# Optimization experiments

Hardware: AMD Instinct MI355X
Metric: run time of the kernel (lower is better)

## Reference

```python
import jax, jax.numpy as jnp
import numpy as np

N_NODES = 100000

def gcn_conv(x, edge_index, W, b):
    # GCNConv with normalize=True and self-loops:
    # out = D^{-1/2} (A + I) D^{-1/2} (x W) + b
    h = x @ W                                   # [N, out]
    src, dst = edge_index[0], edge_index[1]
    deg = jax.ops.segment_sum(jnp.ones(src.shape[0], h.dtype), dst,
                              num_segments=N_NODES) + 1.0  # +1 for self loop
    dinv = jax.lax.rsqrt(deg)
    norm = dinv[src] * dinv[dst]                # [E]
    agg = jax.ops.segment_sum(h[src] * norm[:, None], dst,
                              num_segments=N_NODES)        # [N, out]
    agg = agg + h * (1.0 / deg)[:, None]        # self-loop term: norm_ii = 1/deg_i
    return agg + b


def setup_inputs() -> dict:
    key = jax.random.key(0)
    k0, k1, k2, k3 = jax.random.split(key, 4)
    N, E, F_IN, H, C = N_NODES, 1600000, 256, 128, 40
    x = jax.random.normal(k0, (N, F_IN), dtype=jnp.float32)
    edge_index = jax.random.randint(k1, (2, E), 0, N, dtype=jnp.int64)
    W1 = jax.random.normal(k2, (F_IN, H), dtype=jnp.float32) * (1.0 / np.sqrt(F_IN))
    b1 = jnp.zeros((H,), jnp.float32)
    W2 = jax.random.normal(k3, (H, C), dtype=jnp.float32) * (1.0 / np.sqrt(H))
    b2 = jnp.zeros((C,), jnp.float32)
    return {"x": x, "edge_index": edge_index, "W1": W1, "b1": b1, "W2": W2, "b2": b2}


def reference(x, edge_index, W1, b1, W2, b2):
    # layer 1 + ReLU (dropout = identity in eval mode)
    h = jax.nn.relu(gcn_conv(x, edge_index, W1, b1))
    # final layer (no activation)
    return gcn_conv(h, edge_index, W2, b2)
```

## Files before the change

kernel.cpp:

```cpp
#include <hip/hip_runtime.h>
#include <hip/hip_bf16.h>


#define FIN 256
#define HDIM 128
#define CDIM 40
#define CAP 8192
#define EC 8192

typedef __attribute__((ext_vector_type(8))) short bf16x8;
typedef __attribute__((ext_vector_type(4))) float f32x4;
typedef __attribute__((ext_vector_type(2))) float f32x2;

__device__ inline short f2bf(float f) {
    unsigned u = __float_as_uint(f);
    unsigned r = (u + 0x7FFFu + ((u >> 16) & 1u)) >> 16;
    return (short)r;
}
__device__ inline float bflo(unsigned u) { return __uint_as_float(u << 16); }
__device__ inline float bfhi(unsigned u) { return __uint_as_float(u & 0xFFFF0000u); }
__device__ inline f32x2 unpk(unsigned u) { return (f32x2){bflo(u), bfhi(u)}; }
__device__ inline float ub0(unsigned u) { return (float)(u & 255u); }
__device__ inline float ub1(unsigned u) { return (float)((u >> 8) & 255u); }
__device__ inline float ub2(unsigned u) { return (float)((u >> 16) & 255u); }
__device__ inline float ub3(unsigned u) { return (float)(u >> 24); }

__global__ __launch_bounds__(1024) void scatter_k(const int* __restrict__ ei, int* __restrict__ gcnt,
                                                  int* __restrict__ bmem, int E, int NBUCK) {
    __shared__ int hist[512];
    __shared__ int base[512];
    const int tid = threadIdx.x;
    for (int t = tid; t < NBUCK; t += 1024) hist[t] = 0;
    __syncthreads();
    const int e0 = blockIdx.x * EC;
    const int e1 = min(E, e0 + EC);
    for (int e = e0 + tid; e < e1; e += 1024) atomicAdd(&hist[ei[E + e] >> 8], 1);
    __syncthreads();
    for (int t = tid; t < NBUCK; t += 1024) base[t] = atomicAdd(&gcnt[t], hist[t]);
    __syncthreads();
    for (int e = e0 + tid; e < e1; e += 1024) {
        int s = ei[e];
        int d = ei[E + e];
        int b = d >> 8;
        int pos = atomicAdd(&base[b], 1);
        bmem[b * CAP + pos] = s | ((d & 255) << 20);
    }
}

__global__ __launch_bounds__(256) void p2_build_k(const int* __restrict__ bmem, const int* __restrict__ bcnt,
                                                  int* __restrict__ csr, int2* __restrict__ nseg,
                                                  float* __restrict__ dinv, float* __restrict__ invd,
                                                  const float* __restrict__ W1, const float* __restrict__ W2,
                                                  short* __restrict__ W1T, short* __restrict__ W2T, int N) {
    __shared__ int hist[256], cur[256], sc[256];
    __shared__ int stage[CAP];
    const int b = blockIdx.x;
    const int tid = threadIdx.x;

    for (int idx = b * 256 + tid; idx < FIN * HDIM + 48 * HDIM; idx += gridDim.x * 256) {
        if (idx < FIN * HDIM) {
            int k = idx >> 7, n = idx & 127;
            W1T[n * FIN + k] = f2bf(W1[idx]);
        } else {
            int j = idx - FIN * HDIM;
            int c = j >> 7, k = j & 127;
            W2T[j] = (c < CDIM) ? f2bf(W2[k * CDIM + c]) : (short)0;
        }
    }

    int cnt = bcnt[b];
    if (cnt > CAP) cnt = CAP;
    const int* src = bmem + b * CAP;
    hist[tid] = 0;
    __syncthreads();
    for (int j = tid; j < cnt; j += 256) atomicAdd(&hist[src[j] >> 20], 1);
    __syncthreads();
    int v = hist[tid];
    sc[tid] = v;
    __syncthreads();
    for (int off = 1; off < 256; off <<= 1) {
        int t = (tid >= off) ? sc[tid - off] : 0;
        __syncthreads();
        sc[tid] += t;
        __syncthreads();
    }
    int excl = sc[tid] - v;
    cur[tid] = excl;
    int i = b * 256 + tid;
    if (i < N) {
        nseg[i] = make_int2(b * CAP + excl, v);
        float dg = (float)(v + 1);
        dinv[i] = rsqrtf(dg);
        invd[i] = 1.0f / dg;
    }
    __syncthreads();
    for (int j = tid; j < cnt; j += 256) {
        int rec = src[j];
        int pos = atomicAdd(&cur[rec >> 20], 1);
        stage[pos] = rec & 0xFFFFF;
    }
    __syncthreads();
    int* dst = csr + b * CAP;
    for (int j = tid; j < cnt; j += 256) dst[j] = stage[j];
}

#define LDSTRIDE 40
__global__ __launch_bounds__(256) void gemm1_mfma_k(const float* __restrict__ X,
                                                    const short* __restrict__ W1T,
                                                    const float* __restrict__ dinv,
                                                    unsigned char* __restrict__ T1q,
                                                    float* __restrict__ scl,
                                                    float* __restrict__ wsc, int N) {
    __shared__ short SH[128 * LDSTRIDE * 2];
    short* As = SH;
    short* Bs = SH + 128 * LDSTRIDE;
    const int tid = threadIdx.x;
    const int lane = tid & 63;
    const int wid = tid >> 6;
    const int w0 = wid & 1, w1 = wid >> 1;
    const int quad = lane >> 4;
    const int l16 = lane & 15;
    const int rowbase = blockIdx.x * 128;
    const int sr = tid >> 1;
    const int sh = tid & 1;

    f32x4 acc[4][4];
#pragma unroll
    for (int a = 0; a < 4; a++)
#pragma unroll
        for (int b = 0; b < 4; b++) acc[a][b] = (f32x4){0.f, 0.f, 0.f, 0.f};

    const int arow = min(rowbase + sr, N - 1);
    const float* xsrc = X + (size_t)arow * FIN + sh * 16;
    const int4* bsrc = (const int4*)(W1T + (size_t)sr * FIN + sh * 16);

    for (int k0 = 0; k0 < FIN; k0 += 32) {
        float vals[16];
        *(float4*)&vals[0]  = *(const float4*)(xsrc + k0);
        *(float4*)&vals[4]  = *(const float4*)(xsrc + k0 + 4);
        *(float4*)&vals[8]  = *(const float4*)(xsrc + k0 + 8);
        *(float4*)&vals[12] = *(const float4*)(xsrc + k0 + 12);
        short tmp[16];
#pragma unroll
        for (int c = 0; c < 16; c++) tmp[c] = f2bf(vals[c]);
        ((int4*)&As[sr * LDSTRIDE + sh * 16])[0] = ((int4*)tmp)[0];
        ((int4*)&As[sr * LDSTRIDE + sh * 16])[1] = ((int4*)tmp)[1];
        int4 b0 = bsrc[k0 >> 3];
        int4 b1 = bsrc[(k0 >> 3) + 1];
        ((int4*)&Bs[sr * LDSTRIDE + sh * 16])[0] = b0;
        ((int4*)&Bs[sr * LDSTRIDE + sh * 16])[1] = b1;
        __syncthreads();

        bf16x8 afr[4], bfr[4];
#pragma unroll
        for (int mt = 0; mt < 4; mt++)
            afr[mt] = *(const bf16x8*)&As[(w1 * 64 + mt * 16 + l16) * LDSTRIDE + quad * 8];
#pragma unroll
        for (int nt = 0; nt < 4; nt++)
            bfr[nt] = *(const bf16x8*)&Bs[(w0 * 64 + nt * 16 + l16) * LDSTRIDE + quad * 8];
#pragma unroll
        for (int mt = 0; mt < 4; mt++)
#pragma unroll
            for (int nt = 0; nt < 4; nt++)
                acc[mt][nt] = __builtin_amdgcn_mfma_f32_16x16x32_bf16(afr[mt], bfr[nt], acc[mt][nt], 0, 0, 0);
        __syncthreads();
    }

    unsigned char* qbuf = (unsigned char*)SH;
    float* rmaxb = (float*)((char*)SH + 16384);
#pragma unroll
    for (int mt = 0; mt < 4; mt++) {
#pragma unroll
        for (int r = 0; r < 4; r++) {
            float m = fabsf(acc[mt][0][r]);
            m = fmaxf(m, fabsf(acc[mt][1][r]));
            m = fmaxf(m, fabsf(acc[mt][2][r]));
            m = fmaxf(m, fabsf(acc[mt][3][r]));
#pragma unroll
            for (int off = 1; off < 16; off <<= 1) m = fmaxf(m, __shfl_xor(m, off));
            rmaxb[w0 * 128 + w1 * 64 + mt * 16 + quad * 4 + r] = m;
        }
    }
    __syncthreads();
    if (tid < 128) {
        int grow = rowbase + tid;
        if (grow < N) {
            float rv = fmaxf(rmaxb[tid], rmaxb[128 + tid]);
            float s = rv * (1.f / 127.f);
            scl[grow] = s;
            wsc[grow] = s * dinv[grow];
        }
    }
#pragma unroll
    for (int mt = 0; mt < 4; mt++) {
#pragma unroll
        for (int r = 0; r < 4; r++) {
            const int row = w1 * 64 + mt * 16 + quad * 4 + r;
            float rv = fmaxf(rmaxb[row], rmaxb[128 + row]);
            float qinv = rv > 0.f ? 127.f / rv : 0.f;
#pragma unroll
            for (int nt = 0; nt < 4; nt++) {
                int qi = (int)rintf(acc[mt][nt][r] * qinv) + 128;
                qi = qi < 0 ? 0 : (qi > 255 ? 255 : qi);
                qbuf[row * 128 + w0 * 64 + nt * 16 + l16] = (unsigned char)qi;
            }
        }
    }
    __syncthreads();
#pragma unroll
    for (int it = 0; it < 4; it++) {
        int idx = tid + it * 256;
        int row = idx >> 3;
        if (rowbase + row < N)
            ((uint4*)(T1q + (size_t)(rowbase + row) * 128))[idx & 7] = ((const uint4*)qbuf)[idx];
    }
}

__global__ __launch_bounds__(256) void agg1_k(const unsigned char* __restrict__ T1q, const int2* __restrict__ nseg,
                                              const int* __restrict__ csr, const float* __restrict__ wsc,
                                              const float* __restrict__ scl, const float* __restrict__ dinv,
                                              const float* __restrict__ invd, const float* __restrict__ b1,
                                              unsigned* __restrict__ Hb, int N) {
    const int lane = threadIdx.x & 63;
    const int quad = lane >> 4;
    const int ql = lane & 15;
    const int i = blockIdx.x * 4 + (threadIdx.x >> 6);
    if (i >= N) return;
    const int2 sg = nseg[i];
    const int e0 = sg.x, deg = sg.y;
    int sv = 0; float wv = 0.f;
    if (lane < deg) { sv = csr[e0 + lane]; wv = wsc[sv]; }

    const uint2* rowp = (const uint2*)T1q;
    uint2 us = rowp[i * 16 + ql];
    const float sscale = scl[i];

    f32x2 acc[4]; float asum = 0.f;
#pragma unroll
    for (int t = 0; t < 4; t++) acc[t] = (f32x2){0.f, 0.f};

    const int dmain = deg < 64 ? deg : 64;
    for (int j = 0; j < dmain; j += 16) {
        const int i0 = j + quad, i1 = j + 4 + quad, i2 = j + 8 + quad, i3 = j + 12 + quad;
        int s0 = __shfl(sv, i0); int s1 = __shfl(sv, i1);
        int s2 = __shfl(sv, i2); int s3 = __shfl(sv, i3);
        float w0 = __shfl(wv, i0); float w1 = __shfl(wv, i1);
        float w2 = __shfl(wv, i2); float w3 = __shfl(wv, i3);
        w0 = (i0 < dmain) ? w0 : 0.f;
        w1 = (i1 < dmain) ? w1 : 0.f;
        w2 = (i2 < dmain) ? w2 : 0.f;
        w3 = (i3 < dmain) ? w3 : 0.f;
        uint2 u0 = rowp[s0 * 16 + ql];
        uint2 u1 = rowp[s1 * 16 + ql];
        uint2 u2 = rowp[s2 * 16 + ql];
        uint2 u3 = rowp[s3 * 16 + ql];
        asum += w0 + w1 + w2 + w3;
        f32x2 W0 = (f32x2){w0, w0}, W1v = (f32x2){w1, w1}, W2v = (f32x2){w2, w2}, W3v = (f32x2){w3, w3};
        acc[0] += W0 * (f32x2){ub0(u0.x), ub1(u0.x)} + W1v * (f32x2){ub0(u1.x), ub1(u1.x)}
                + W2v * (f32x2){ub0(u2.x), ub1(u2.x)} + W3v * (f32x2){ub0(u3.x), ub1(u3.x)};
        acc[1] += W0 * (f32x2){ub2(u0.x), ub3(u0.x)} + W1v * (f32x2){ub2(u1.x), ub3(u1.x)}
                + W2v * (f32x2){ub2(u2.x), ub3(u2.x)} + W3v * (f32x2){ub2(u3.x), ub3(u3.x)};
        acc[2] += W0 * (f32x2){ub0(u0.y), ub1(u0.y)} + W1v * (f32x2){ub0(u1.y), ub1(u1.y)}
                + W2v * (f32x2){ub0(u2.y), ub1(u2.y)} + W3v * (f32x2){ub0(u3.y), ub1(u3.y)};
        acc[3] += W0 * (f32x2){ub2(u0.y), ub3(u0.y)} + W1v * (f32x2){ub2(u1.y), ub3(u1.y)}
                + W2v * (f32x2){ub2(u2.y), ub3(u2.y)} + W3v * (f32x2){ub2(u3.y), ub3(u3.y)};
    }
    const int eEnd = e0 + deg;
    for (int e = e0 + 64; e < eEnd; e += 4) {
        int idx = e + quad;
        int cl = idx < eEnd ? idx : eEnd - 1;
        int sj = csr[cl];
        float wj = (idx < eEnd) ? wsc[sj] : 0.f;
        uint2 u = rowp[sj * 16 + ql];
        asum += wj;
        f32x2 Wj = (f32x2){wj, wj};
        acc[0] += Wj * (f32x2){ub0(u.x), ub1(u.x)};
        acc[1] += Wj * (f32x2){ub2(u.x), ub3(u.x)};
        acc[2] += Wj * (f32x2){ub0(u.y), ub1(u.y)};
        acc[3] += Wj * (f32x2){ub2(u.y), ub3(u.y)};
    }
#pragma unroll
    for (int t = 0; t < 4; t++) {
        acc[t].x += __shfl_xor(acc[t].x, 16); acc[t].y += __shfl_xor(acc[t].y, 16);
        acc[t].x += __shfl_xor(acc[t].x, 32); acc[t].y += __shfl_xor(acc[t].y, 32);
    }
    asum += __shfl_xor(asum, 16);
    asum += __shfl_xor(asum, 32);

    const float di = dinv[i];
    const float sf2 = invd[i] * sscale;
    const float K = -128.f * (sf2 + di * asum);
    float4 bA = *(const float4*)(b1 + ql * 8);
    float4 bB = *(const float4*)(b1 + ql * 8 + 4);
    float o0 = fmaxf(bA.x + sf2 * ub0(us.x) + di * acc[0].x + K, 0.f);
    float o1 = fmaxf(bA.y + sf2 * ub1(us.x) + di * acc[0].y + K, 0.f);
    float o2 = fmaxf(bA.z + sf2 * ub2(us.x) + di * acc[1].x + K, 0.f);
    float o3 = fmaxf(bA.w + sf2 * ub3(us.x) + di * acc[1].y + K, 0.f);
    float o4 = fmaxf(bB.x + sf2 * ub0(us.y) + di * acc[2].x + K, 0.f);
    float o5 = fmaxf(bB.y + sf2 * ub1(us.y) + di * acc[2].y + K, 0.f);
    float o6 = fmaxf(bB.z + sf2 * ub2(us.y) + di * acc[3].x + K, 0.f);
    float o7 = fmaxf(bB.w + sf2 * ub3(us.y) + di * acc[3].y + K, 0.f);
    uint4 pk;
    pk.x = ((unsigned)(unsigned short)f2bf(o0)) | (((unsigned)(unsigned short)f2bf(o1)) << 16);
    pk.y = ((unsigned)(unsigned short)f2bf(o2)) | (((unsigned)(unsigned short)f2bf(o3)) << 16);
    pk.z = ((unsigned)(unsigned short)f2bf(o4)) | (((unsigned)(unsigned short)f2bf(o5)) << 16);
    pk.w = ((unsigned)(unsigned short)f2bf(o6)) | (((unsigned)(unsigned short)f2bf(o7)) << 16);
    if (quad == 0) ((uint4*)(Hb + (size_t)i * 64))[ql] = pk;
}

__global__ __launch_bounds__(256) void gemm2_mfma_k(const short* __restrict__ Hb,
                                                    const short* __restrict__ W2T,
                                                    const float* __restrict__ dinv,
                                                    unsigned char* __restrict__ T2q,
                                                    float* __restrict__ scl2,
                                                    float* __restrict__ wsc2, int N) {
    __shared__ short As[128 * LDSTRIDE];
    __shared__ short Bs[48 * LDSTRIDE];
    const int tid = threadIdx.x;
    const int lane = tid & 63;
    const int wid = tid >> 6;
    const int quad = lane >> 4;
    const int l16 = lane & 15;
    const int rowbase = blockIdx.x * 128;
    const int sr = tid >> 1;
    const int sh = tid & 1;

    f32x4 acc[2][3];
#pragma unroll
    for (int a = 0; a < 2; a++)
#pragma unroll
        for (int b = 0; b < 3; b++) acc[a][b] = (f32x4){0.f, 0.f, 0.f, 0.f};

    const int arow = min(rowbase + sr, N - 1);
    const int4* asrc = (const int4*)(Hb + (size_t)arow * HDIM + sh * 16);
    const int br = tid >> 1, bh = tid & 1;
    const int4* bsrc = (const int4*)(W2T + br * HDIM + bh * 16);

    for (int k0 = 0; k0 < HDIM; k0 += 32) {
        int4 a0 = asrc[k0 >> 3];
        int4 a1 = asrc[(k0 >> 3) + 1];
        ((int4*)&As[sr * LDSTRIDE + sh * 16])[0] = a0;
        ((int4*)&As[sr * LDSTRIDE + sh * 16])[1] = a1;
        if (tid < 96) {
            int4 b0 = bsrc[k0 >> 3];
            int4 b1 = bsrc[(k0 >> 3) + 1];
            ((int4*)&Bs[br * LDSTRIDE + bh * 16])[0] = b0;
            ((int4*)&Bs[br * LDSTRIDE + bh * 16])[1] = b1;
        }
        __syncthreads();
        bf16x8 afr[2], bfr[3];
#pragma unroll
        for (int mt = 0; mt < 2; mt++)
            afr[mt] = *(const bf16x8*)&As[(wid * 32 + mt * 16 + l16) * LDSTRIDE + quad * 8];
#pragma unroll
        for (int nt = 0; nt < 3; nt++)
            bfr[nt] = *(const bf16x8*)&Bs[(nt * 16 + l16) * LDSTRIDE + quad * 8];
#pragma unroll
        for (int mt = 0; mt < 2; mt++)
#pragma unroll
            for (int nt = 0; nt < 3; nt++)
                acc[mt][nt] = __builtin_amdgcn_mfma_f32_16x16x32_bf16(afr[mt], bfr[nt], acc[mt][nt], 0, 0, 0);
        __syncthreads();
    }

    unsigned char* qbuf = (unsigned char*)As;
#pragma unroll
    for (int mt = 0; mt < 2; mt++) {
#pragma unroll
        for (int r = 0; r < 4; r++) {
            float m = fmaxf(fmaxf(fabsf(acc[mt][0][r]), fabsf(acc[mt][1][r])), fabsf(acc[mt][2][r]));
#pragma unroll
            for (int off = 1; off < 16; off <<= 1) m = fmaxf(m, __shfl_xor(m, off));
            const int row = wid * 32 + mt * 16 + quad * 4 + r;
            const int grow = rowbase + row;
            const float qinv = m > 0.f ? 127.f / m : 0.f;
            if (l16 == 0 && grow < N) {
                float s = m * (1.f / 127.f);
                scl2[grow] = s;
                wsc2[grow] = s * dinv[grow];
            }
            int q0 = (int)rintf(acc[mt][0][r] * qinv) + 128;
            int q1 = (int)rintf(acc[mt][1][r] * qinv) + 128;
            int q2 = (int)rintf(acc[mt][2][r] * qinv) + 128;
            q0 = q0 < 0 ? 0 : (q0 > 255 ? 255 : q0);
            q1 = q1 < 0 ? 0 : (q1 > 255 ? 255 : q1);
            q2 = q2 < 0 ? 0 : (q2 > 255 ? 255 : q2);
            qbuf[row * 64 + l16]      = (unsigned char)q0;
            qbuf[row * 64 + 16 + l16] = (unsigned char)q1;
            qbuf[row * 64 + 32 + l16] = (unsigned char)q2;
        }
    }
    for (int idx = tid; idx < 2048; idx += 256)
        qbuf[(idx >> 4) * 64 + 48 + (idx & 15)] = (unsigned char)128;
    __syncthreads();
#pragma unroll
    for (int it = 0; it < 2; it++) {
        int idx = tid + it * 256;
        int row = idx >> 2;
        if (rowbase + row < N)
            ((uint4*)(T2q + (size_t)(rowbase + row) * 64))[idx & 3] = ((const uint4*)qbuf)[idx];
    }
}

__global__ __launch_bounds__(256) void agg2_k(const unsigned char* __restrict__ T2q, const int2* __restrict__ nseg,
                                              const int* __restrict__ csr, const float* __restrict__ wsc2,
                                              const float* __restrict__ scl2, const float* __restrict__ dinv,
                                              const float* __restrict__ invd, const float* __restrict__ b2,
                                              float* __restrict__ OUT, int N) {
    const int lane = threadIdx.x & 63;
    const int oct = lane >> 3;
    const int olr = lane & 7;
    const int i = blockIdx.x * 4 + (threadIdx.x >> 6);
    if (i >= N) return;
    const int2 sg = nseg[i];
    const int e0 = sg.x, deg = sg.y;
    int sv = 0; float wv = 0.f;
    if (lane < deg) { sv = csr[e0 + lane]; wv = wsc2[sv]; }

    const uint2* rowp = (const uint2*)T2q;
    uint2 us = rowp[i * 8 + olr];
    const float sscale = scl2[i];

    f32x2 acc[4]; float asum = 0.f;
#pragma unroll
    for (int t = 0; t < 4; t++) acc[t] = (f32x2){0.f, 0.f};

    const int dmain = deg < 64 ? deg : 64;
    for (int j = 0; j < dmain; j += 16) {
        const int i0 = j + oct, i1 = j + 8 + oct;
        int s0 = __shfl(sv, i0); int s1 = __shfl(sv, i1);
        float w0 = __shfl(wv, i0); float w1 = __shfl(wv, i1);
        w0 = (i0 < dmain) ? w0 : 0.f;
        w1 = (i1 < dmain) ? w1 : 0.f;
        uint2 u0 = rowp[s0 * 8 + olr];
        uint2 u1 = rowp[s1 * 8 + olr];
        asum += w0 + w1;
        f32x2 W0 = (f32x2){w0, w0}, W1v = (f32x2){w1, w1};
        acc[0] += W0 * (f32x2){ub0(u0.x), ub1(u0.x)} + W1v * (f32x2){ub0(u1.x), ub1(u1.x)};
        acc[1] += W0 * (f32x2){ub2(u0.x), ub3(u0.x)} + W1v * (f32x2){ub2(u1.x), ub3(u1.x)};
        acc[2] += W0 * (f32x2){ub0(u0.y), ub1(u0.y)} + W1v * (f32x2){ub0(u1.y), ub1(u1.y)};
        acc[3] += W0 * (f32x2){ub2(u0.y), ub3(u0.y)} + W1v * (f32x2){ub2(u1.y), ub3(u1.y)};
    }
    const int eEnd = e0 + deg;
    for (int e = e0 + 64; e < eEnd; e += 8) {
        int idx = e + oct;
        int cl = idx < eEnd ? idx : eEnd - 1;
        int sj = csr[cl];
        float wj = (idx < eEnd) ? wsc2[sj] : 0.f;
        uint2 u = rowp[sj * 8 + olr];
        asum += wj;
        f32x2 Wj = (f32x2){wj, wj};
        acc[0] += Wj * (f32x2){ub0(u.x), ub1(u.x)};
        acc[1] += Wj * (f32x2){ub2(u.x), ub3(u.x)};
        acc[2] += Wj * (f32x2){ub0(u.y), ub1(u.y)};
        acc[3] += Wj * (f32x2){ub2(u.y), ub3(u.y)};
    }
#pragma unroll
    for (int t = 0; t < 4; t++) {
        acc[t].x += __shfl_xor(acc[t].x, 8);  acc[t].y += __shfl_xor(acc[t].y, 8);
        acc[t].x += __shfl_xor(acc[t].x, 16); acc[t].y += __shfl_xor(acc[t].y, 16);
        acc[t].x += __shfl_xor(acc[t].x, 32); acc[t].y += __shfl_xor(acc[t].y, 32);
    }
    asum += __shfl_xor(asum, 8);
    asum += __shfl_xor(asum, 16);
    asum += __shfl_xor(asum, 32);

    if (oct == 0 && olr < 5) {
        const float di = dinv[i];
        const float sf2 = invd[i] * sscale;
        const float K = -128.f * (sf2 + di * asum);
        float4 bA = *(const float4*)(b2 + olr * 8);
        float4 bB = *(const float4*)(b2 + olr * 8 + 4);
        float4 oA, oB;
        oA.x = bA.x + sf2 * ub0(us.x) + di * acc[0].x + K;
        oA.y = bA.y + sf2 * ub1(us.x) + di * acc[0].y + K;
        oA.z = bA.z + sf2 * ub2(us.x) + di * acc[1].x + K;
        oA.w = bA.w + sf2 * ub3(us.x) + di * acc[1].y + K;
        oB.x = bB.x + sf2 * ub0(us.y) + di * acc[2].x + K;
        oB.y = bB.y + sf2 * ub1(us.y) + di * acc[2].y + K;
        oB.z = bB.z + sf2 * ub2(us.y) + di * acc[3].x + K;
        oB.w = bB.w + sf2 * ub3(us.y) + di * acc[3].y + K;
        *(float4*)(OUT + (size_t)i * CDIM + olr * 8) = oA;
        *(float4*)(OUT + (size_t)i * CDIM + olr * 8 + 4) = oB;
    }
}

extern "C" void kernel_launch(void* const* d_in, const int* in_sizes, int n_in,
                              void* d_out, int out_size, void* d_ws, size_t ws_size,
                              hipStream_t stream) {
    const float* x   = (const float*)d_in[0];
    const int*   ei  = (const int*)d_in[1];
    const float* W1  = (const float*)d_in[2];
    const float* b1  = (const float*)d_in[3];
    const float* W2  = (const float*)d_in[4];
    const float* b2  = (const float*)d_in[5];
    float*       out = (float*)d_out;

    const int Hd  = in_sizes[3];
    const int Fin = in_sizes[2] / Hd;
    const int N   = in_sizes[0] / Fin;
    const int E   = in_sizes[1] / 2;

    const int NBUCK = (N + 255) / 256;
    const int NB1   = (E + EC - 1) / EC;

    char* base = (char*)d_ws;
    size_t off = 0;
    auto alloc = [&](size_t bytes) -> void* {
        void* p = base + off;
        off += (bytes + 255) & ~(size_t)255;
        return p;
    };
    size_t bmemB = (size_t)NBUCK * CAP * 4;
    size_t t1qB  = (size_t)N * 128;
    size_t regA  = bmemB > t1qB ? bmemB : t1qB;
    char* pA = (char*)alloc(regA);
    int*           bmem = (int*)pA;
    unsigned char* t1q  = (unsigned char*)pA;

    int*      gcnt = (int*)alloc((size_t)NBUCK * 4);
    int*      csr  = (int*)alloc((size_t)NBUCK * CAP * 4);
    int2*     nseg = (int2*)alloc((size_t)N * 8);
    float*    dinv = (float*)alloc((size_t)N * 4);
    float*    invd = (float*)alloc((size_t)N * 4);
    float*    scl  = (float*)alloc((size_t)N * 4);
    float*    wsc  = (float*)alloc((size_t)N * 4);
    float*    scl2 = (float*)alloc((size_t)N * 4);
    float*    wsc2 = (float*)alloc((size_t)N * 4);
    short*    W1T  = (short*)alloc((size_t)HDIM * FIN * 2);
    short*    W2T  = (short*)alloc((size_t)48 * HDIM * 2);
    unsigned* hb   = (unsigned*)alloc((size_t)N * HDIM * 2);
    unsigned char* t2q = (unsigned char*)alloc((size_t)N * 64);

    hipMemsetAsync(gcnt, 0, (size_t)NBUCK * 4, stream);
    scatter_k<<<NB1, 1024, 0, stream>>>(ei, gcnt, bmem, E, NBUCK);
    p2_build_k<<<NBUCK, 256, 0, stream>>>(bmem, gcnt, csr, nseg, dinv, invd, W1, W2, W1T, W2T, N);

    gemm1_mfma_k<<<(N + 127) / 128, 256, 0, stream>>>(x, W1T, dinv, t1q, scl, wsc, N);
    agg1_k<<<(N + 3) / 4, 256, 0, stream>>>(t1q, nseg, csr, wsc, scl, dinv, invd, b1, hb, N);
    gemm2_mfma_k<<<(N + 127) / 128, 256, 0, stream>>>((const short*)hb, W2T, dinv, t2q, scl2, wsc2, N);
    agg2_k<<<(N + 3) / 4, 256, 0, stream>>>(t2q, nseg, csr, wsc2, scl2, dinv, invd, b2, out, N);
}
```

Before: 326.1 us.

## Replace bucketed CSR build with global degree count, scan, and atomic fill

Replaces the two-pass bucketed scatter (fixed-capacity per-bucket staging plus an LDS sort) with three simpler kernels. The first counts degrees with global atomics, the second does a per-block scan with an atomic global offset, and the third fills the CSR with per-destination atomic cursors. This removes the capacity-limited staging buffer and its extra read/write pass, at the cost of many global atomics and a neighbor order within each row that is no longer deterministic. The row order now depends on block completion order, which changes memory locality for the aggregation kernels. The GEMM1 fp32-to-bf16 conversion also switches to the packed intrinsic.

```diff
diff --git a/kernel.cpp b/kernel.cpp
--- a/kernel.cpp
+++ b/kernel.cpp
@@ -5,8 +5,6 @@
 #define FIN 256
 #define HDIM 128
 #define CDIM 40
-#define CAP 8192
-#define EC 8192
 
 typedef __attribute__((ext_vector_type(8))) short bf16x8;
 typedef __attribute__((ext_vector_type(4))) float f32x4;
@@ -25,35 +23,18 @@
 __device__ inline float ub2(unsigned u) { return (float)((u >> 16) & 255u); }
 __device__ inline float ub3(unsigned u) { return (float)(u >> 24); }
 
-__global__ __launch_bounds__(1024) void scatter_k(const int* __restrict__ ei, int* __restrict__ gcnt,
-                                                  int* __restrict__ bmem, int E, int NBUCK) {
-    __shared__ int hist[512];
-    __shared__ int base[512];
-    const int tid = threadIdx.x;
-    for (int t = tid; t < NBUCK; t += 1024) hist[t] = 0;
-    __syncthreads();
-    const int e0 = blockIdx.x * EC;
-    const int e1 = min(E, e0 + EC);
-    for (int e = e0 + tid; e < e1; e += 1024) atomicAdd(&hist[ei[E + e] >> 8], 1);
-    __syncthreads();
-    for (int t = tid; t < NBUCK; t += 1024) base[t] = atomicAdd(&gcnt[t], hist[t]);
-    __syncthreads();
-    for (int e = e0 + tid; e < e1; e += 1024) {
-        int s = ei[e];
-        int d = ei[E + e];
-        int b = d >> 8;
-        int pos = atomicAdd(&base[b], 1);
-        bmem[b * CAP + pos] = s | ((d & 255) << 20);
-    }
-}
-
-__global__ __launch_bounds__(256) void p2_build_k(const int* __restrict__ bmem, const int* __restrict__ bcnt,
-                                                  int* __restrict__ csr, int2* __restrict__ nseg,
-                                                  float* __restrict__ dinv, float* __restrict__ invd,
-                                                  const float* __restrict__ W1, const float* __restrict__ W2,
-                                                  short* __restrict__ W1T, short* __restrict__ W2T, int N) {
-    __shared__ int hist[256], cur[256], sc[256];
-    __shared__ int stage[CAP];
+__global__ __launch_bounds__(1024) void deg_k(const int* __restrict__ ei, int* __restrict__ deg, int E) {
+    int e = blockIdx.x * 1024 + threadIdx.x;
+    if (e < E) atomicAdd(&deg[ei[E + e]], 1);
+}
+
+__global__ __launch_bounds__(256) void alloc_k(const int* __restrict__ deg, int* __restrict__ total,
+                                               int2* __restrict__ nseg, int* __restrict__ cur,
+                                               float* __restrict__ dinv, float* __restrict__ invd,
+                                               const float* __restrict__ W1, const float* __restrict__ W2,
+                                               short* __restrict__ W1T, short* __restrict__ W2T, int N) {
+    __shared__ int sc[256];
+    __shared__ int bbase;
     const int b = blockIdx.x;
     const int tid = threadIdx.x;
 
@@ -68,14 +49,8 @@
         }
     }
 
-    int cnt = bcnt[b];
-    if (cnt > CAP) cnt = CAP;
-    const int* src = bmem + b * CAP;
-    hist[tid] = 0;
-    __syncthreads();
-    for (int j = tid; j < cnt; j += 256) atomicAdd(&hist[src[j] >> 20], 1);
-    __syncthreads();
-    int v = hist[tid];
+    const int i = b * 256 + tid;
+    const int v = (i < N) ? deg[i] : 0;
     sc[tid] = v;
     __syncthreads();
     for (int off = 1; off < 256; off <<= 1) {
@@ -84,24 +59,29 @@
         sc[tid] += t;
         __syncthreads();
     }
-    int excl = sc[tid] - v;
-    cur[tid] = excl;
-    int i = b * 256 + tid;
+    const int incl = sc[tid];
+    const int excl = incl - v;
+    if (tid == 255) bbase = atomicAdd(total, incl);
+    __syncthreads();
+    const int base = bbase;
     if (i < N) {
-        nseg[i] = make_int2(b * CAP + excl, v);
+        nseg[i] = make_int2(base + excl, v);
+        cur[i] = base + excl;
         float dg = (float)(v + 1);
         dinv[i] = rsqrtf(dg);
         invd[i] = 1.0f / dg;
     }
-    __syncthreads();
-    for (int j = tid; j < cnt; j += 256) {
-        int rec = src[j];
-        int pos = atomicAdd(&cur[rec >> 20], 1);
-        stage[pos] = rec & 0xFFFFF;
-    }
-    __syncthreads();
-    int* dst = csr + b * CAP;
-    for (int j = tid; j < cnt; j += 256) dst[j] = stage[j];
+}
+
+__global__ __launch_bounds__(1024) void fill_k(const int* __restrict__ ei, int* __restrict__ cur,
+                                               int* __restrict__ csr, int E) {
+    int e = blockIdx.x * 1024 + threadIdx.x;
+    if (e < E) {
+        int s = ei[e];
+        int d = ei[E + e];
+        int pos = atomicAdd(&cur[d], 1);
+        csr[pos] = s;
+    }
 }
 
 #define LDSTRIDE 40
@@ -140,11 +120,12 @@
         *(float4*)&vals[4]  = *(const float4*)(xsrc + k0 + 4);
         *(float4*)&vals[8]  = *(const float4*)(xsrc + k0 + 8);
         *(float4*)&vals[12] = *(const float4*)(xsrc + k0 + 12);
-        short tmp[16];
-#pragma unroll
-        for (int c = 0; c < 16; c++) tmp[c] = f2bf(vals[c]);
-        ((int4*)&As[sr * LDSTRIDE + sh * 16])[0] = ((int4*)tmp)[0];
-        ((int4*)&As[sr * LDSTRIDE + sh * 16])[1] = ((int4*)tmp)[1];
+        __hip_bfloat162 tmp2[8];
+#pragma unroll
+        for (int c = 0; c < 8; c++)
+            tmp2[c] = __float22bfloat162_rn(make_float2(vals[2 * c], vals[2 * c + 1]));
+        ((int4*)&As[sr * LDSTRIDE + sh * 16])[0] = ((int4*)tmp2)[0];
+        ((int4*)&As[sr * LDSTRIDE + sh * 16])[1] = ((int4*)tmp2)[1];
         int4 b0 = bsrc[k0 >> 3];
         int4 b1 = bsrc[(k0 >> 3) + 1];
         ((int4*)&Bs[sr * LDSTRIDE + sh * 16])[0] = b0;
@@ -502,7 +483,7 @@
     const int E   = in_sizes[1] / 2;
 
     const int NBUCK = (N + 255) / 256;
-    const int NB1   = (E + EC - 1) / EC;
+    const int NBE   = (E + 1023) / 1024;
 
     char* base = (char*)d_ws;
     size_t off = 0;
@@ -511,15 +492,10 @@
         off += (bytes + 255) & ~(size_t)255;
         return p;
     };
-    size_t bmemB = (size_t)NBUCK * CAP * 4;
-    size_t t1qB  = (size_t)N * 128;
-    size_t regA  = bmemB > t1qB ? bmemB : t1qB;
-    char* pA = (char*)alloc(regA);
-    int*           bmem = (int*)pA;
-    unsigned char* t1q  = (unsigned char*)pA;
-
-    int*      gcnt = (int*)alloc((size_t)NBUCK * 4);
-    int*      csr  = (int*)alloc((size_t)NBUCK * CAP * 4);
+    unsigned char* t1q  = (unsigned char*)alloc((size_t)N * 128);
+    int*      deg  = (int*)alloc(((size_t)N + 64) * 4);
+    int*      cur  = (int*)alloc((size_t)N * 4);
+    int*      csr  = (int*)alloc((size_t)E * 4);
     int2*     nseg = (int2*)alloc((size_t)N * 8);
     float*    dinv = (float*)alloc((size_t)N * 4);
     float*    invd = (float*)alloc((size_t)N * 4);
@@ -531,10 +507,12 @@
     short*    W2T  = (short*)alloc((size_t)48 * HDIM * 2);
     unsigned* hb   = (unsigned*)alloc((size_t)N * HDIM * 2);
     unsigned char* t2q = (unsigned char*)alloc((size_t)N * 64);
-
-    hipMemsetAsync(gcnt, 0, (size_t)NBUCK * 4, stream);
-    scatter_k<<<NB1, 1024, 0, stream>>>(ei, gcnt, bmem, E, NBUCK);
-    p2_build_k<<<NBUCK, 256, 0, stream>>>(bmem, gcnt, csr, nseg, dinv, invd, W1, W2, W1T, W2T, N);
+    int* total = deg + N;
+
+    hipMemsetAsync(deg, 0, ((size_t)N + 64) * 4, stream);
+    deg_k<<<NBE, 1024, 0, stream>>>(ei, deg, E);
+    alloc_k<<<NBUCK, 256, 0, stream>>>(deg, total, nseg, cur, dinv, invd, W1, W2, W1T, W2T, N);
+    fill_k<<<NBE, 1024, 0, stream>>>(ei, cur, csr, E);
 
     gemm1_mfma_k<<<(N + 127) / 128, 256, 0, stream>>>(x, W1T, dinv, t1q, scl, wsc, N);
     agg1_k<<<(N + 3) / 4, 256, 0, stream>>>(t1q, nseg, csr, wsc, scl, dinv, invd, b1, hb, N);
```

Measured after the change: 470.8 us. 44.4% more time.

## Regroup agg2 lanes to 16 per row with 4-byte loads; use bf16x2 conversion

Applied to the files above, without the earlier changes.

The layer-2 aggregation kernel now assigns 16 lanes per neighbor row, each loading 4 bytes of the 64-byte quantized row, so one wavefront processes four neighbors per step instead of eight lanes per row with 8-byte loads. This changes how many rows are gathered concurrently, halves the per-lane accumulators and drops one shuffle-reduction stage. Separately, the GEMM's fp32-to-bf16 conversion now uses the paired __float22bfloat162_rn intrinsic instead of manual per-element rounding, which may map to a packed convert instruction. Narrower per-lane loads mean more load instructions per byte gathered.

```diff
diff --git a/kernel.cpp b/kernel.cpp
--- a/kernel.cpp
+++ b/kernel.cpp
@@ -140,11 +140,12 @@
         *(float4*)&vals[4]  = *(const float4*)(xsrc + k0 + 4);
         *(float4*)&vals[8]  = *(const float4*)(xsrc + k0 + 8);
         *(float4*)&vals[12] = *(const float4*)(xsrc + k0 + 12);
-        short tmp[16];
-#pragma unroll
-        for (int c = 0; c < 16; c++) tmp[c] = f2bf(vals[c]);
-        ((int4*)&As[sr * LDSTRIDE + sh * 16])[0] = ((int4*)tmp)[0];
-        ((int4*)&As[sr * LDSTRIDE + sh * 16])[1] = ((int4*)tmp)[1];
+        __hip_bfloat162 tmp2[8];
+#pragma unroll
+        for (int c = 0; c < 8; c++)
+            tmp2[c] = __float22bfloat162_rn(make_float2(vals[2 * c], vals[2 * c + 1]));
+        ((int4*)&As[sr * LDSTRIDE + sh * 16])[0] = ((int4*)tmp2)[0];
+        ((int4*)&As[sr * LDSTRIDE + sh * 16])[1] = ((int4*)tmp2)[1];
         int4 b0 = bsrc[k0 >> 3];
         int4 b1 = bsrc[(k0 >> 3) + 1];
         ((int4*)&Bs[sr * LDSTRIDE + sh * 16])[0] = b0;
@@ -408,8 +409,8 @@
                                               const float* __restrict__ invd, const float* __restrict__ b2,
                                               float* __restrict__ OUT, int N) {
     const int lane = threadIdx.x & 63;
-    const int oct = lane >> 3;
-    const int olr = lane & 7;
+    const int quad = lane >> 4;
+    const int ql = lane & 15;
     const int i = blockIdx.x * 4 + (threadIdx.x >> 6);
     if (i >= N) return;
     const int2 sg = nseg[i];
@@ -417,71 +418,67 @@
     int sv = 0; float wv = 0.f;
     if (lane < deg) { sv = csr[e0 + lane]; wv = wsc2[sv]; }
 
-    const uint2* rowp = (const uint2*)T2q;
-    uint2 us = rowp[i * 8 + olr];
+    const unsigned* rowp = (const unsigned*)T2q;
+    unsigned us = rowp[i * 16 + ql];
     const float sscale = scl2[i];
 
-    f32x2 acc[4]; float asum = 0.f;
-#pragma unroll
-    for (int t = 0; t < 4; t++) acc[t] = (f32x2){0.f, 0.f};
+    f32x2 acc[2]; float asum = 0.f;
+    acc[0] = (f32x2){0.f, 0.f};
+    acc[1] = (f32x2){0.f, 0.f};
 
     const int dmain = deg < 64 ? deg : 64;
     for (int j = 0; j < dmain; j += 16) {
-        const int i0 = j + oct, i1 = j + 8 + oct;
+        const int i0 = j + quad, i1 = j + 4 + quad, i2 = j + 8 + quad, i3 = j + 12 + quad;
         int s0 = __shfl(sv, i0); int s1 = __shfl(sv, i1);
+        int s2 = __shfl(sv, i2); int s3 = __shfl(sv, i3);
         float w0 = __shfl(wv, i0); float w1 = __shfl(wv, i1);
+        float w2 = __shfl(wv, i2); float w3 = __shfl(wv, i3);
         w0 = (i0 < dmain) ? w0 : 0.f;
         w1 = (i1 < dmain) ? w1 : 0.f;
-        uint2 u0 = rowp[s0 * 8 + olr];
-        uint2 u1 = rowp[s1 * 8 + olr];
-        asum += w0 + w1;
-        f32x2 W0 = (f32x2){w0, w0}, W1v = (f32x2){w1, w1};
-        acc[0] += W0 * (f32x2){ub0(u0.x), ub1(u0.x)} + W1v * (f32x2){ub0(u1.x), ub1(u1.x)};
-        acc[1] += W0 * (f32x2){ub2(u0.x), ub3(u0.x)} + W1v * (f32x2){ub2(u1.x), ub3(u1.x)};
-        acc[2] += W0 * (f32x2){ub0(u0.y), ub1(u0.y)} + W1v * (f32x2){ub0(u1.y), ub1(u1.y)};
-        acc[3] += W0 * (f32x2){ub2(u0.y), ub3(u0.y)} + W1v * (f32x2){ub2(u1.y), ub3(u1.y)};
+        w2 = (i2 < dmain) ? w2 : 0.f;
+        w3 = (i3 < dmain) ? w3 : 0.f;
+        unsigned u0 = rowp[s0 * 16 + ql];
+        unsigned u1 = rowp[s1 * 16 + ql];
+        unsigned u2 = rowp[s2 * 16 + ql];
+        unsigned u3 = rowp[s3 * 16 + ql];
+        asum += w0 + w1 + w2 + w3;
+        f32x2 W0 = (f32x2){w0, w0}, W1v = (f32x2){w1, w1}, W2v = (f32x2){w2, w2}, W3v = (f32x2){w3, w3};
+        acc[0] += W0 * (f32x2){ub0(u0), ub1(u0)} + W1v * (f32x2){ub0(u1), ub1(u1)}
+                + W2v * (f32x2){ub0(u2), ub1(u2)} + W3v * (f32x2){ub0(u3), ub1(u3)};
+        acc[1] += W0 * (f32x2){ub2(u0), ub3(u0)} + W1v * (f32x2){ub2(u1), ub3(u1)}
+                + W2v * (f32x2){ub2(u2), ub3(u2)} + W3v * (f32x2){ub2(u3), ub3(u3)};
     }
     const int eEnd = e0 + deg;
-    for (int e = e0 + 64; e < eEnd; e += 8) {
-        int idx = e + oct;
+    for (int e = e0 + 64; e < eEnd; e += 4) {
+        int idx = e + quad;
         int cl = idx < eEnd ? idx : eEnd - 1;
         int sj = csr[cl];
         float wj = (idx < eEnd) ? wsc2[sj] : 0.f;
-        uint2 u = rowp[sj * 8 + olr];
+        unsigned u = rowp[sj * 16 + ql];
         asum += wj;
         f32x2 Wj = (f32x2){wj, wj};
-        acc[0] += Wj * (f32x2){ub0(u.x), ub1(u.x)};
-        acc[1] += Wj * (f32x2){ub2(u.x), ub3(u.x)};
-        acc[2] += Wj * (f32x2){ub0(u.y), ub1(u.y)};
-        acc[3] += Wj * (f32x2){ub2(u.y), ub3(u.y)};
-    }
-#pragma unroll
-    for (int t = 0; t < 4; t++) {
-        acc[t].x += __shfl_xor(acc[t].x, 8);  acc[t].y += __shfl_xor(acc[t].y, 8);
+        acc[0] += Wj * (f32x2){ub0(u), ub1(u)};
+        acc[1] += Wj * (f32x2){ub2(u), ub3(u)};
+    }
+#pragma unroll
+    for (int t = 0; t < 2; t++) {
         acc[t].x += __shfl_xor(acc[t].x, 16); acc[t].y += __shfl_xor(acc[t].y, 16);
         acc[t].x += __shfl_xor(acc[t].x, 32); acc[t].y += __shfl_xor(acc[t].y, 32);
     }
-    asum += __shfl_xor(asum, 8);
     asum += __shfl_xor(asum, 16);
     asum += __shfl_xor(asum, 32);
 
-    if (oct == 0 && olr < 5) {
+    if (quad == 0 && ql < 10) {
         const float di = dinv[i];
         const float sf2 = invd[i] * sscale;
         const float K = -128.f * (sf2 + di * asum);
-        float4 bA = *(const float4*)(b2 + olr * 8);
-        float4 bB = *(const float4*)(b2 + olr * 8 + 4);
-        float4 oA, oB;
-        oA.x = bA.x + sf2 * ub0(us.x) + di * acc[0].x + K;
-        oA.y = bA.y + sf2 * ub1(us.x) + di * acc[0].y + K;
-        oA.z = bA.z + sf2 * ub2(us.x) + di * acc[1].x + K;
-        oA.w = bA.w + sf2 * ub3(us.x) + di * acc[1].y + K;
-        oB.x = bB.x + sf2 * ub0(us.y) + di * acc[2].x + K;
-        oB.y = bB.y + sf2 * ub1(us.y) + di * acc[2].y + K;
-        oB.z = bB.z + sf2 * ub2(us.y) + di * acc[3].x + K;
-        oB.w = bB.w + sf2 * ub3(us.y) + di * acc[3].y + K;
-        *(float4*)(OUT + (size_t)i * CDIM + olr * 8) = oA;
-        *(float4*)(OUT + (size_t)i * CDIM + olr * 8 + 4) = oB;
+        float4 bb = *(const float4*)(b2 + ql * 4);
+        float4 o;
+        o.x = bb.x + sf2 * ub0(us) + di * acc[0].x + K;
+        o.y = bb.y + sf2 * ub1(us) + di * acc[0].y + K;
+        o.z = bb.z + sf2 * ub2(us) + di * acc[1].x + K;
+        o.w = bb.w + sf2 * ub3(us) + di * acc[1].y + K;
+        *(float4*)(OUT + (size_t)i * CDIM + ql * 4) = o;
     }
 }
 
```

After: 318.8 us. -2.2%, faster.
